# Performance work log

Hardware: AMD Instinct MI355X
Metric: run time of the kernel (lower is better)

Reference implementation:

```python
import jax, jax.numpy as jnp
import numpy as np

D2 = 200  # 2*100 hardcoded in BiAttentionLayer.__init__
NEG = -10000000.0


def masked_softmax(v, m):
    # Faithful to the torch masked_softmax: softmax(v * m), re-mask, renormalize.
    r = jax.nn.softmax(v * m, axis=-1)
    r = r * m
    return r / (jnp.sum(r, axis=-1, keepdims=True) + 1e-13)


def setup_inputs() -> dict:
    key = jax.random.key(0)
    k0, k1, k2, k3, k4, k5 = jax.random.split(key, 6)
    N, T, J = 64, 1024, 64
    H = jax.random.normal(k0, (N, T, D2), jnp.float32)
    U = jax.random.normal(k1, (N, J, D2), jnp.float32)
    c_mask = jax.random.randint(k2, (N, T), 0, 2).astype(jnp.float32)
    q_mask = jax.random.randint(k3, (N, J), 0, 2).astype(jnp.float32)
    w = jax.random.normal(k4, (3 * D2,), jnp.float32) * 0.05  # Linear(3*d2, 1) weight
    b = jax.random.normal(k5, (), jnp.float32) * 0.05          # Linear bias
    return {"H": H, "U": U, "c_mask": c_mask, "q_mask": q_mask, "w": w, "b": b}


def reference(H, U, c_mask, q_mask, w, b):
    # Similarity: linear over concat(h, u, h*u) decomposed so the (N,T,J,3d)
    # intermediate is never materialized (same math as the torch module).
    w_h, w_u, w_hu = w[:D2], w[D2:2 * D2], w[2 * D2:]
    S = ((H @ w_h)[:, :, None]
         + (U @ w_u)[:, None, :]
         + jnp.einsum('ntd,njd->ntj', H * w_hu, U)
         + b)  # [N,T,J]

    # C2Q: masked softmax over question dim, attend over U.
    S_t = masked_softmax(S, q_mask[:, None, :])        # [N,T,J]
    U_ = jnp.einsum('ntj,njd->ntd', S_t, U)            # [N,T,d2]

    # Q2C: replace masked values with -1e7, max over J, softmax over context dim.
    qm = q_mask[:, None, :]
    S_rep = S * qm + NEG * (1.0 - qm)                  # [N,T,J]
    S_max = jnp.max(S_rep, axis=-1)                    # [N,T]
    a = masked_softmax(S_max, c_mask)                  # [N,T]
    H_ = jnp.einsum('nt,ntd->nd', a, H)[:, None, :]    # [N,1,d2] (broadcasts over T)

    G = jnp.concatenate([H, U_, H * U_, H * H_], axis=-1)  # [N,T,4*d2]
    return G
```

## Files before the change

### kernel.cpp

```cpp
#include <hip/hip_runtime.h>
#include <stdint.h>

#define NEGV -10000000.0f

typedef __attribute__((ext_vector_type(8))) short short8;
typedef __attribute__((ext_vector_type(4))) float f32x4;

__device__ __forceinline__ ushort f2b(float f) {
    uint32_t x = __float_as_uint(f);
    uint32_t r = x + 0x7FFFu + ((x >> 16) & 1u);
    return (ushort)(r >> 16);
}

__launch_bounds__(256)
__global__ void k0_prep(const float* __restrict__ Ug, const float* __restrict__ wg,
                        const float* __restrict__ bg,
                        ushort* __restrict__ BhatW, ushort* __restrict__ UTW,
                        float* __restrict__ cW) {
    __shared__ __align__(16) float sU[64][200];
    __shared__ float sW[600];
    const int tid = threadIdx.x, lane = tid & 63, wid = tid >> 6;
    const int n = blockIdx.x;

    for (int i = tid; i < 600; i += 256) sW[i] = wg[i];
    for (int r = wid; r < 64; r += 4) {
        const float* urow = Ug + (size_t)(n * 64 + r) * 200;
        if (lane < 50) *(float4*)&sU[r][lane * 4] = *(const float4*)(urow + lane * 4);
    }
    __syncthreads();
    const float bval = bg[0];

    ushort* utn = UTW + (size_t)n * 224 * 64;
    for (int d = wid; d < 224; d += 4)
        utn[d * 64 + lane] = (d < 200) ? f2b(sU[lane][d]) : (ushort)0;

    ushort* bhn = BhatW + (size_t)n * 64 * 224;
    for (int r = wid; r < 64; r += 4) {
        float part = 0.f;
        for (int d = lane; d < 224; d += 64) {
            float bh = 0.f;
            if (d < 200) {
                float u = sU[r][d];
                bh = u * sW[400 + d] + sW[d];
                part += u * sW[200 + d];
            }
            bhn[r * 224 + d] = f2b(bh);
        }
        #pragma unroll
        for (int off = 32; off >= 1; off >>= 1) part += __shfl_xor(part, off);
        if (lane == 0) cW[n * 64 + r] = part + bval;
    }
}

__launch_bounds__(256, 3)
__global__ void k1_gemm1_softmax(const float* __restrict__ Hg,
                                 const ushort* __restrict__ BhatW,
                                 const float* __restrict__ cW,
                                 const float* __restrict__ qmg,
                                 ushort* __restrict__ Pws,
                                 float* __restrict__ SmaxWs) {
    __shared__ ushort sP[64][72];
    const int tid = threadIdx.x, lane = tid & 63, wid = tid >> 6;
    const int g = lane >> 4, li = lane & 15;
    const int n = blockIdx.y, t0 = blockIdx.x * 64;

    const float*  Hrow = Hg + (size_t)(n * 1024 + t0 + 16 * wid + li) * 200;
    const ushort* Bn   = BhatW + (size_t)n * 64 * 224;

    f32x4 acc[4];
    #pragma unroll
    for (int jt = 0; jt < 4; ++jt) acc[jt] = (f32x4){0.f, 0.f, 0.f, 0.f};

    #pragma unroll
    for (int kc = 0; kc < 7; ++kc) {
        short8 av;
        if (kc < 6 || g == 0) {
            float4 h0 = *(const float4*)(Hrow + kc * 32 + g * 8);
            float4 h1 = *(const float4*)(Hrow + kc * 32 + g * 8 + 4);
            av[0] = (short)f2b(h0.x); av[1] = (short)f2b(h0.y);
            av[2] = (short)f2b(h0.z); av[3] = (short)f2b(h0.w);
            av[4] = (short)f2b(h1.x); av[5] = (short)f2b(h1.y);
            av[6] = (short)f2b(h1.z); av[7] = (short)f2b(h1.w);
        } else {
            av = (short8){0, 0, 0, 0, 0, 0, 0, 0};
        }
        #pragma unroll
        for (int jt = 0; jt < 4; ++jt) {
            short8 bv = *(const short8*)(Bn + (size_t)(jt * 16 + li) * 224 + kc * 32 + g * 8);
            acc[jt] = __builtin_amdgcn_mfma_f32_16x16x32_bf16(av, bv, acc[jt], 0, 0, 0);
        }
    }

    float cj[4], qm[4];
    #pragma unroll
    for (int jt = 0; jt < 4; ++jt) {
        cj[jt] = cW[n * 64 + jt * 16 + li];
        qm[jt] = qmg[n * 64 + jt * 16 + li];
    }

    #pragma unroll
    for (int reg = 0; reg < 4; ++reg) {
        float x[4], y[4];
        float xm = -1e30f, ym = -1e30f;
        #pragma unroll
        for (int jt = 0; jt < 4; ++jt) {
            float s = acc[jt][reg] + cj[jt];
            x[jt] = s * qm[jt];
            y[jt] = (qm[jt] != 0.f) ? s : NEGV;
            xm = fmaxf(xm, x[jt]); ym = fmaxf(ym, y[jt]);
        }
        #pragma unroll
        for (int off = 1; off <= 8; off <<= 1) {
            xm = fmaxf(xm, __shfl_xor(xm, off));
            ym = fmaxf(ym, __shfl_xor(ym, off));
        }
        float e[4], z = 0.f, zm = 0.f;
        #pragma unroll
        for (int jt = 0; jt < 4; ++jt) {
            e[jt] = __expf(x[jt] - xm);
            z += e[jt]; zm += e[jt] * qm[jt];
        }
        #pragma unroll
        for (int off = 1; off <= 8; off <<= 1) {
            z  += __shfl_xor(z, off);
            zm += __shfl_xor(zm, off);
        }
        float inv = 1.f / (zm + 1e-13f * z);
        int trow = 16 * wid + g * 4 + reg;
        #pragma unroll
        for (int jt = 0; jt < 4; ++jt) sP[trow][jt * 16 + li] = f2b(e[jt] * qm[jt] * inv);
        if (li == 0) SmaxWs[n * 1024 + t0 + trow] = ym;
    }
    __syncthreads();

    uint* pout = (uint*)Pws;
    for (int idx = tid; idx < 2048; idx += 256) {
        int r = idx >> 5, c2 = idx & 31;
        uint v = *(const uint*)&sP[r][c2 * 2];
        pout[(size_t)(n * 1024 + t0 + r) * 32 + c2] = v;
    }
}

__launch_bounds__(256)
__global__ void k2a_softmaxT(const float* __restrict__ cmg,
                             const float* __restrict__ SmaxWs,
                             float* __restrict__ aWs,
                             float* __restrict__ HbarWs) {
    __shared__ float red[8];
    const int tid = threadIdx.x, lane = tid & 63, wid = tid >> 6;
    const int n = blockIdx.x;

    float x[4], m[4];
    #pragma unroll
    for (int i = 0; i < 4; ++i) {
        int t = tid + 256 * i;
        float v = SmaxWs[n * 1024 + t];
        m[i] = cmg[(size_t)n * 1024 + t];
        x[i] = v * m[i];
    }
    float mx = fmaxf(fmaxf(x[0], x[1]), fmaxf(x[2], x[3]));
    #pragma unroll
    for (int off = 32; off >= 1; off >>= 1) mx = fmaxf(mx, __shfl_xor(mx, off));
    if (lane == 0) red[wid] = mx;
    __syncthreads();
    float M = fmaxf(fmaxf(red[0], red[1]), fmaxf(red[2], red[3]));
    __syncthreads();
    float e[4], z = 0.f, zm = 0.f;
    #pragma unroll
    for (int i = 0; i < 4; ++i) {
        e[i] = __expf(x[i] - M);
        z += e[i]; zm += e[i] * m[i];
    }
    #pragma unroll
    for (int off = 32; off >= 1; off >>= 1) {
        z  += __shfl_xor(z, off);
        zm += __shfl_xor(zm, off);
    }
    if (lane == 0) { red[wid] = z; red[4 + wid] = zm; }
    __syncthreads();
    float Z  = red[0] + red[1] + red[2] + red[3];
    float Zm = red[4] + red[5] + red[6] + red[7];
    float inv = 1.f / (Zm + 1e-13f * Z);
    #pragma unroll
    for (int i = 0; i < 4; ++i) aWs[n * 1024 + tid + 256 * i] = e[i] * m[i] * inv;
    if (tid < 200) HbarWs[n * 200 + tid] = 0.f;
}

__launch_bounds__(256)
__global__ void k2b_hbar(const float* __restrict__ Hg,
                         const float* __restrict__ aWs,
                         float* __restrict__ HbarWs) {
    __shared__ float sA[64];
    const int tid = threadIdx.x;
    const int n = blockIdx.y, t0 = blockIdx.x * 64;
    if (tid < 64) sA[tid] = aWs[n * 1024 + t0 + tid];
    __syncthreads();
    if (tid < 200) {
        const float* hp = Hg + (size_t)(n * 1024 + t0) * 200 + tid;
        float acc = 0.f;
        #pragma unroll 8
        for (int t = 0; t < 64; ++t) acc += sA[t] * hp[(size_t)t * 200];
        atomicAdd(HbarWs + n * 200 + tid, acc);
    }
}

__launch_bounds__(256, 3)
__global__ void k3_gemm2_out(const float* __restrict__ Hg,
                             const ushort* __restrict__ UTW,
                             const ushort* __restrict__ Pws,
                             const float* __restrict__ HbarWs,
                             float* __restrict__ Gout) {
    __shared__ __align__(16) float sU2[64][204];
    __shared__ __align__(16) float sHb[200];
    const int tid = threadIdx.x, lane = tid & 63, wid = tid >> 6;
    const int g = lane >> 4, li = lane & 15;
    const int n = blockIdx.y, t0 = blockIdx.x * 64;

    if (tid < 200) sHb[tid] = HbarWs[n * 200 + tid];

    const ushort* Prow = Pws + (size_t)(n * 1024 + t0 + 16 * wid + li) * 64;
    const ushort* UTn  = UTW + (size_t)n * 224 * 64;

    f32x4 acc[13];
    #pragma unroll
    for (int dt = 0; dt < 13; ++dt) acc[dt] = (f32x4){0.f, 0.f, 0.f, 0.f};

    #pragma unroll
    for (int kc = 0; kc < 2; ++kc) {
        short8 av = *(const short8*)(Prow + kc * 32 + g * 8);
        #pragma unroll
        for (int dt = 0; dt < 13; ++dt) {
            short8 bv = *(const short8*)(UTn + (size_t)(dt * 16 + li) * 64 + kc * 32 + g * 8);
            acc[dt] = __builtin_amdgcn_mfma_f32_16x16x32_bf16(av, bv, acc[dt], 0, 0, 0);
        }
    }

    #pragma unroll
    for (int dt = 0; dt < 13; ++dt) {
        int d = dt * 16 + li;
        if (d < 200) {
            #pragma unroll
            for (int reg = 0; reg < 4; ++reg)
                sU2[16 * wid + g * 4 + reg][d] = acc[dt][reg];
        }
    }
    __syncthreads();

    for (int r = wid; r < 64; r += 4) {
        const float* hrow = Hg + (size_t)(n * 1024 + t0 + r) * 200;
        float* orow = Gout + (size_t)(n * 1024 + t0 + r) * 800;
        if (lane < 50) {
            int d0 = lane * 4;
            f32x4 h  = *(const f32x4*)(hrow + d0);
            f32x4 u  = *(const f32x4*)&sU2[r][d0];
            f32x4 hb = *(const f32x4*)&sHb[d0];
            f32x4 hu = h * u;
            f32x4 hh = h * hb;
            __builtin_nontemporal_store(h,  (f32x4*)(orow + d0));
            __builtin_nontemporal_store(u,  (f32x4*)(orow + 200 + d0));
            __builtin_nontemporal_store(hu, (f32x4*)(orow + 400 + d0));
            __builtin_nontemporal_store(hh, (f32x4*)(orow + 600 + d0));
        }
    }
}

extern "C" void kernel_launch(void* const* d_in, const int* in_sizes, int n_in,
                              void* d_out, int out_size, void* d_ws, size_t ws_size,
                              hipStream_t stream) {
    (void)in_sizes; (void)n_in; (void)out_size; (void)ws_size;
    const float* Hg  = (const float*)d_in[0];
    const float* Ug  = (const float*)d_in[1];
    const float* cmg = (const float*)d_in[2];
    const float* qmg = (const float*)d_in[3];
    const float* wg  = (const float*)d_in[4];
    const float* bg  = (const float*)d_in[5];
    float* Gout = (float*)d_out;

    char* ws = (char*)d_ws;
    ushort* Pws    = (ushort*)(ws);
    float*  SmaxWs = (float*) (ws + 8388608);
    float*  aWs    = (float*) (ws + 8650752);
    float*  HbarWs = (float*) (ws + 8912896);
    float*  cWs    = (float*) (ws + 8964096);
    ushort* BhatWs = (ushort*)(ws + 8980480);
    ushort* UTWs   = (ushort*)(ws + 10815488);

    dim3 blk(256, 1, 1);
    k0_prep<<<dim3(64, 1, 1), blk, 0, stream>>>(Ug, wg, bg, BhatWs, UTWs, cWs);
    k1_gemm1_softmax<<<dim3(16, 64, 1), blk, 0, stream>>>(Hg, BhatWs, cWs, qmg, Pws, SmaxWs);
    k2a_softmaxT<<<dim3(64, 1, 1), blk, 0, stream>>>(cmg, SmaxWs, aWs, HbarWs);
    k2b_hbar<<<dim3(16, 64, 1), blk, 0, stream>>>(Hg, aWs, HbarWs);
    k3_gemm2_out<<<dim3(16, 64, 1), blk, 0, stream>>>(Hg, UTWs, Pws, HbarWs, Gout);
}
```

Measured before the change: 324.6 us.

## Fuse similarity GEMM, softmax and attention GEMM into one single-wave kernel

Merges the first GEMM plus row softmax with the second GEMM that forms U_, so P stays in LDS instead of round-tripping through a workspace. Each fused block is one 64-thread wave over 16 rows, and it writes the H, U_ and H*U_ parts of G early. A separate lightweight kernel writes only the H*Hbar segment once Hbar is ready. U_ is now staged in LDS as bf16, which adds rounding error to the output. H is read an extra time by the new kernel, and the small single-wave blocks may lower per-block efficiency.

```diff
diff --git a/kernel.cpp b/kernel.cpp
--- a/kernel.cpp
+++ b/kernel.cpp
@@ -11,13 +11,16 @@
     uint32_t r = x + 0x7FFFu + ((x >> 16) & 1u);
     return (ushort)(r >> 16);
 }
+__device__ __forceinline__ float b2f(ushort u) {
+    union { float f; uint32_t i; } v; v.i = ((uint32_t)u) << 16; return v.f;
+}
 
 __launch_bounds__(256)
 __global__ void k0_prep(const float* __restrict__ Ug, const float* __restrict__ wg,
                         const float* __restrict__ bg,
                         ushort* __restrict__ BhatW, ushort* __restrict__ UTW,
                         float* __restrict__ cW) {
-    __shared__ __align__(16) float sU[64][200];
+    __shared__ __align__(16) float sU[64][204];
     __shared__ float sW[600];
     const int tid = threadIdx.x, lane = tid & 63, wid = tid >> 6;
     const int n = blockIdx.x;
@@ -52,42 +55,46 @@
     }
 }
 
-__launch_bounds__(256, 3)
-__global__ void k1_gemm1_softmax(const float* __restrict__ Hg,
-                                 const ushort* __restrict__ BhatW,
-                                 const float* __restrict__ cW,
-                                 const float* __restrict__ qmg,
-                                 ushort* __restrict__ Pws,
-                                 float* __restrict__ SmaxWs) {
-    __shared__ ushort sP[64][72];
-    const int tid = threadIdx.x, lane = tid & 63, wid = tid >> 6;
+__launch_bounds__(64)
+__global__ void k13_fused(const float* __restrict__ Hg,
+                          const ushort* __restrict__ BhatW,
+                          const float* __restrict__ cW,
+                          const float* __restrict__ qmg,
+                          const ushort* __restrict__ UTW,
+                          float* __restrict__ SmaxWs,
+                          float* __restrict__ Gout) {
+    __shared__ ushort sP[16][76];
+    __shared__ ushort sU2[16][204];
+    const int lane = threadIdx.x;
     const int g = lane >> 4, li = lane & 15;
-    const int n = blockIdx.y, t0 = blockIdx.x * 64;
-
-    const float*  Hrow = Hg + (size_t)(n * 1024 + t0 + 16 * wid + li) * 200;
+    const int n = blockIdx.y, t0 = blockIdx.x * 16;
+
+    const float*  Hrow = Hg + (size_t)(n * 1024 + t0 + li) * 200;
     const ushort* Bn   = BhatW + (size_t)n * 64 * 224;
 
-    f32x4 acc[4];
-    #pragma unroll
-    for (int jt = 0; jt < 4; ++jt) acc[jt] = (f32x4){0.f, 0.f, 0.f, 0.f};
-
+    short8 av[7];
     #pragma unroll
     for (int kc = 0; kc < 7; ++kc) {
-        short8 av;
         if (kc < 6 || g == 0) {
             float4 h0 = *(const float4*)(Hrow + kc * 32 + g * 8);
             float4 h1 = *(const float4*)(Hrow + kc * 32 + g * 8 + 4);
-            av[0] = (short)f2b(h0.x); av[1] = (short)f2b(h0.y);
-            av[2] = (short)f2b(h0.z); av[3] = (short)f2b(h0.w);
-            av[4] = (short)f2b(h1.x); av[5] = (short)f2b(h1.y);
-            av[6] = (short)f2b(h1.z); av[7] = (short)f2b(h1.w);
+            av[kc][0] = (short)f2b(h0.x); av[kc][1] = (short)f2b(h0.y);
+            av[kc][2] = (short)f2b(h0.z); av[kc][3] = (short)f2b(h0.w);
+            av[kc][4] = (short)f2b(h1.x); av[kc][5] = (short)f2b(h1.y);
+            av[kc][6] = (short)f2b(h1.z); av[kc][7] = (short)f2b(h1.w);
         } else {
-            av = (short8){0, 0, 0, 0, 0, 0, 0, 0};
-        }
+            av[kc] = (short8){0, 0, 0, 0, 0, 0, 0, 0};
+        }
+    }
+    f32x4 acc[4];
+    #pragma unroll
+    for (int jt = 0; jt < 4; ++jt) acc[jt] = (f32x4){0.f, 0.f, 0.f, 0.f};
+    #pragma unroll
+    for (int kc = 0; kc < 7; ++kc) {
         #pragma unroll
         for (int jt = 0; jt < 4; ++jt) {
             short8 bv = *(const short8*)(Bn + (size_t)(jt * 16 + li) * 224 + kc * 32 + g * 8);
-            acc[jt] = __builtin_amdgcn_mfma_f32_16x16x32_bf16(av, bv, acc[jt], 0, 0, 0);
+            acc[jt] = __builtin_amdgcn_mfma_f32_16x16x32_bf16(av[kc], bv, acc[jt], 0, 0, 0);
         }
     }
 
@@ -97,7 +104,6 @@
         cj[jt] = cW[n * 64 + jt * 16 + li];
         qm[jt] = qmg[n * 64 + jt * 16 + li];
     }
-
     #pragma unroll
     for (int reg = 0; reg < 4; ++reg) {
         float x[4], y[4];
@@ -126,18 +132,51 @@
             zm += __shfl_xor(zm, off);
         }
         float inv = 1.f / (zm + 1e-13f * z);
-        int trow = 16 * wid + g * 4 + reg;
+        int trow = g * 4 + reg;
         #pragma unroll
         for (int jt = 0; jt < 4; ++jt) sP[trow][jt * 16 + li] = f2b(e[jt] * qm[jt] * inv);
         if (li == 0) SmaxWs[n * 1024 + t0 + trow] = ym;
     }
-    __syncthreads();
-
-    uint* pout = (uint*)Pws;
-    for (int idx = tid; idx < 2048; idx += 256) {
-        int r = idx >> 5, c2 = idx & 31;
-        uint v = *(const uint*)&sP[r][c2 * 2];
-        pout[(size_t)(n * 1024 + t0 + r) * 32 + c2] = v;
+
+    const ushort* UTn = UTW + (size_t)n * 224 * 64;
+    f32x4 acc2[13];
+    #pragma unroll
+    for (int dt = 0; dt < 13; ++dt) acc2[dt] = (f32x4){0.f, 0.f, 0.f, 0.f};
+    #pragma unroll
+    for (int kc = 0; kc < 2; ++kc) {
+        short8 a2 = *(const short8*)(&sP[li][kc * 32 + g * 8]);
+        #pragma unroll
+        for (int dt = 0; dt < 13; ++dt) {
+            short8 bv = *(const short8*)(UTn + (size_t)(dt * 16 + li) * 64 + kc * 32 + g * 8);
+            acc2[dt] = __builtin_amdgcn_mfma_f32_16x16x32_bf16(a2, bv, acc2[dt], 0, 0, 0);
+        }
+    }
+
+    #pragma unroll
+    for (int dt = 0; dt < 13; ++dt) {
+        int d = dt * 16 + li;
+        if (d < 200) {
+            #pragma unroll
+            for (int reg = 0; reg < 4; ++reg)
+                sU2[g * 4 + reg][d] = f2b(acc2[dt][reg]);
+        }
+    }
+
+    for (int r = 0; r < 16; ++r) {
+        if (lane < 50) {
+            int d0 = lane * 4;
+            const float* hrow = Hg + (size_t)(n * 1024 + t0 + r) * 200;
+            float* orow = Gout + (size_t)(n * 1024 + t0 + r) * 800;
+            f32x4 h = *(const f32x4*)(hrow + d0);
+            uint2 uraw = *(const uint2*)&sU2[r][d0];
+            f32x4 u;
+            u[0] = b2f((ushort)(uraw.x & 0xffffu)); u[1] = b2f((ushort)(uraw.x >> 16));
+            u[2] = b2f((ushort)(uraw.y & 0xffffu)); u[3] = b2f((ushort)(uraw.y >> 16));
+            f32x4 hu = h * u;
+            __builtin_nontemporal_store(h,  (f32x4*)(orow + d0));
+            __builtin_nontemporal_store(u,  (f32x4*)(orow + 200 + d0));
+            __builtin_nontemporal_store(hu, (f32x4*)(orow + 400 + d0));
+        }
     }
 }
 
@@ -204,61 +243,23 @@
     }
 }
 
-__launch_bounds__(256, 3)
-__global__ void k3_gemm2_out(const float* __restrict__ Hg,
-                             const ushort* __restrict__ UTW,
-                             const ushort* __restrict__ Pws,
-                             const float* __restrict__ HbarWs,
-                             float* __restrict__ Gout) {
-    __shared__ __align__(16) float sU2[64][204];
+__launch_bounds__(256)
+__global__ void k4_hh(const float* __restrict__ Hg,
+                      const float* __restrict__ HbarWs,
+                      float* __restrict__ Gout) {
     __shared__ __align__(16) float sHb[200];
     const int tid = threadIdx.x, lane = tid & 63, wid = tid >> 6;
-    const int g = lane >> 4, li = lane & 15;
     const int n = blockIdx.y, t0 = blockIdx.x * 64;
-
     if (tid < 200) sHb[tid] = HbarWs[n * 200 + tid];
-
-    const ushort* Prow = Pws + (size_t)(n * 1024 + t0 + 16 * wid + li) * 64;
-    const ushort* UTn  = UTW + (size_t)n * 224 * 64;
-
-    f32x4 acc[13];
-    #pragma unroll
-    for (int dt = 0; dt < 13; ++dt) acc[dt] = (f32x4){0.f, 0.f, 0.f, 0.f};
-
-    #pragma unroll
-    for (int kc = 0; kc < 2; ++kc) {
-        short8 av = *(const short8*)(Prow + kc * 32 + g * 8);
-        #pragma unroll
-        for (int dt = 0; dt < 13; ++dt) {
-            short8 bv = *(const short8*)(UTn + (size_t)(dt * 16 + li) * 64 + kc * 32 + g * 8);
-            acc[dt] = __builtin_amdgcn_mfma_f32_16x16x32_bf16(av, bv, acc[dt], 0, 0, 0);
-        }
-    }
-
-    #pragma unroll
-    for (int dt = 0; dt < 13; ++dt) {
-        int d = dt * 16 + li;
-        if (d < 200) {
-            #pragma unroll
-            for (int reg = 0; reg < 4; ++reg)
-                sU2[16 * wid + g * 4 + reg][d] = acc[dt][reg];
-        }
-    }
-    __syncthreads();
-
+    __syncthreads();
     for (int r = wid; r < 64; r += 4) {
-        const float* hrow = Hg + (size_t)(n * 1024 + t0 + r) * 200;
-        float* orow = Gout + (size_t)(n * 1024 + t0 + r) * 800;
         if (lane < 50) {
             int d0 = lane * 4;
+            const float* hrow = Hg + (size_t)(n * 1024 + t0 + r) * 200;
+            float* orow = Gout + (size_t)(n * 1024 + t0 + r) * 800;
             f32x4 h  = *(const f32x4*)(hrow + d0);
-            f32x4 u  = *(const f32x4*)&sU2[r][d0];
             f32x4 hb = *(const f32x4*)&sHb[d0];
-            f32x4 hu = h * u;
             f32x4 hh = h * hb;
-            __builtin_nontemporal_store(h,  (f32x4*)(orow + d0));
-            __builtin_nontemporal_store(u,  (f32x4*)(orow + 200 + d0));
-            __builtin_nontemporal_store(hu, (f32x4*)(orow + 400 + d0));
             __builtin_nontemporal_store(hh, (f32x4*)(orow + 600 + d0));
         }
     }
@@ -277,18 +278,18 @@
     float* Gout = (float*)d_out;
 
     char* ws = (char*)d_ws;
-    ushort* Pws    = (ushort*)(ws);
-    float*  SmaxWs = (float*) (ws + 8388608);
-    float*  aWs    = (float*) (ws + 8650752);
-    float*  HbarWs = (float*) (ws + 8912896);
-    float*  cWs    = (float*) (ws + 8964096);
-    ushort* BhatWs = (ushort*)(ws + 8980480);
-    ushort* UTWs   = (ushort*)(ws + 10815488);
-
-    dim3 blk(256, 1, 1);
-    k0_prep<<<dim3(64, 1, 1), blk, 0, stream>>>(Ug, wg, bg, BhatWs, UTWs, cWs);
-    k1_gemm1_softmax<<<dim3(16, 64, 1), blk, 0, stream>>>(Hg, BhatWs, cWs, qmg, Pws, SmaxWs);
-    k2a_softmaxT<<<dim3(64, 1, 1), blk, 0, stream>>>(cmg, SmaxWs, aWs, HbarWs);
-    k2b_hbar<<<dim3(16, 64, 1), blk, 0, stream>>>(Hg, aWs, HbarWs);
-    k3_gemm2_out<<<dim3(16, 64, 1), blk, 0, stream>>>(Hg, UTWs, Pws, HbarWs, Gout);
-}
+    float*  SmaxWs = (float*) (ws);
+    float*  aWs    = (float*) (ws + 262144);
+    float*  HbarWs = (float*) (ws + 524288);
+    float*  cWs    = (float*) (ws + 575488);
+    ushort* BhatWs = (ushort*)(ws + 591872);
+    ushort* UTWs   = (ushort*)(ws + 2426880);
+
+    dim3 blk256(256, 1, 1);
+    k0_prep<<<dim3(64, 1, 1), blk256, 0, stream>>>(Ug, wg, bg, BhatWs, UTWs, cWs);
+    k13_fused<<<dim3(64, 64, 1), dim3(64, 1, 1), 0, stream>>>(Hg, BhatWs, cWs, qmg,
+                                                              UTWs, SmaxWs, Gout);
+    k2a_softmaxT<<<dim3(64, 1, 1), blk256, 0, stream>>>(cmg, SmaxWs, aWs, HbarWs);
+    k2b_hbar<<<dim3(16, 64, 1), blk256, 0, stream>>>(Hg, aWs, HbarWs);
+    k4_hh<<<dim3(16, 64, 1), blk256, 0, stream>>>(Hg, HbarWs, Gout);
+}
```

Result: no change. 325.9 us (+0.4%).
